# Optimization experiments

Hardware: AMD Instinct MI355X
Metric: run time of the kernel (lower is better)

Reference implementation:

```python
import jax, jax.numpy as jnp
import numpy as np

SIDE = 32
N_NODES = SIDE * SIDE          # n_nodes = 1024
WIDTH = 128
IN_DIM = 128
T_DIM = 2
U_DIM = 1
BATCH = 8
MSG_STEPS = int(np.sqrt(N_NODES))  # 32
LN_EPS = 1e-5


def _create_grid():
    # matches GEN.create_grid for t_dim == 2
    pos = np.array([[i / (SIDE - 1), j / (SIDE - 1)]
                    for i in range(SIDE) for j in range(SIDE)], dtype=np.float32)
    edges = []
    for i in range(1, SIDE):
        for j in range(1, SIDE):
            a = SIDE * i + j
            b = SIDE * (i - 1) + j
            c = SIDE * i + (j - 1)
            edges += [[a, b], [b, a], [c, a], [a, c]]
    edge_index = np.array(edges, dtype=np.int64).T  # [2, E]
    return pos, edge_index


def setup_inputs() -> dict:
    key = jax.random.key(0)
    ks = jax.random.split(key, 16)
    node_pos_np, edge_index_np = _create_grid()

    def lin(k, fan_in, fan_out):
        kw, kb = jax.random.split(k)
        bound = 1.0 / np.sqrt(fan_in)
        W = jax.random.uniform(kw, (fan_in, fan_out), jnp.float32, -bound, bound)
        b = jax.random.uniform(kb, (fan_out,), jnp.float32, -bound, bound)
        return W, b

    We1, be1 = lin(ks[0], IN_DIM, WIDTH)
    We2, be2 = lin(ks[1], WIDTH, WIDTH)
    We3, be3 = lin(ks[2], WIDTH, WIDTH)
    Wg, bg = lin(ks[3], WIDTH + T_DIM, WIDTH)
    Wd1, bd1 = lin(ks[4], WIDTH + T_DIM, WIDTH)
    Wd2, bd2 = lin(ks[5], WIDTH, WIDTH)
    Wd3, bd3 = lin(ks[6], WIDTH, U_DIM)

    return {
        'X1': jax.random.uniform(ks[7], (BATCH, IN_DIM + T_DIM), jnp.float32),
        'node_pos': jnp.asarray(node_pos_np),
        'edge_index': jnp.asarray(edge_index_np),
        'We1': We1, 'be1': be1, 'We2': We2, 'be2': be2, 'We3': We3, 'be3': be3,
        'Wg': Wg, 'bg': bg,
        'gamma': jnp.ones((WIDTH,), jnp.float32),
        'beta': jnp.zeros((WIDTH,), jnp.float32),
        'Wd1': Wd1, 'bd1': bd1, 'Wd2': Wd2, 'bd2': bd2, 'Wd3': Wd3, 'bd3': bd3,
    }


def _gen_forward(X1, node_pos, edge_index, We1, be1, We2, be2, We3, be3,
                 Wg, bg, gamma, beta, Wd1, bd1, Wd2, bd2, Wd3, bd3):
    s, t = X1[:, :-T_DIM], X1[:, -T_DIM:]

    # encoder MLP: Linear-ReLU-Linear-ReLU-Linear
    h = jax.nn.relu(s @ We1 + be1)
    h = jax.nn.relu(h @ We2 + be2)
    enc = h @ We3 + be3                                   # [B, W]

    # per-sample graph construction: softmax over node distance to origin
    # (identical for every sample), node_features = weight @ enc[i][None,:]
    d0 = jnp.sqrt(jnp.sum(node_pos ** 2, axis=1, keepdims=True))  # [N,1]
    w0 = jax.nn.softmax(-d0, axis=0)                              # [N,1]
    x = w0[None, :, :] * enc[:, None, :]                          # [B,N,W]

    # GCNConv normalization with added self-loops (symmetric norm)
    row, col = edge_index[0], edge_index[1]
    deg = jnp.ones((N_NODES,), x.dtype).at[col].add(1.0)
    dinv = deg ** -0.5
    enorm = dinv[row] * dinv[col]   # edge norm
    snorm = dinv * dinv             # self-loop norm
    posb = jnp.broadcast_to(node_pos[None], (x.shape[0], N_NODES, T_DIM))

    def step(xc, _):
        xin = jnp.concatenate([posb, xc], axis=-1)        # [B,N,W+2]
        xw = xin @ Wg                                     # [B,N,W]
        msgs = enorm[None, :, None] * xw[:, row, :]       # [B,E,W]
        agg = (snorm[None, :, None] * xw).at[:, col, :].add(msgs) + bg
        xn = xc + agg
        mu = jnp.mean(xn, axis=-1, keepdims=True)
        var = jnp.var(xn, axis=-1, keepdims=True)
        xn = (xn - mu) * jax.lax.rsqrt(var + LN_EPS) * gamma + beta
        return xn, None

    x, _ = jax.lax.scan(step, x, None, length=MSG_STEPS)  # [B,N,W]

    # readout: softmax over node distance to query point t
    dist = jnp.sqrt(jnp.sum((node_pos[None] - t[:, None, :]) ** 2,
                            axis=2, keepdims=True))       # [B,N,1]
    wt = jax.nn.softmax(-dist, axis=1)                    # [B,N,1]
    hidden = jnp.einsum('bnk,bnw->bw', wt, x)             # [B,W]
    hidden = jnp.concatenate([hidden, t], axis=1)

    h = jax.nn.relu(hidden @ Wd1 + bd1)
    h = jax.nn.relu(h @ Wd2 + bd2)
    y = (h @ Wd3 + bd3).squeeze()                         # [B] (u_dim == 1)
    return y


def reference(X1, node_pos, edge_index, We1, be1, We2, be2, We3, be3,
              Wg, bg, gamma, beta, Wd1, bd1, Wd2, bd2, Wd3, bd3):
    return _gen_forward(X1, node_pos, edge_index, We1, be1, We2, be2, We3, be3,
                        Wg, bg, gamma, beta, Wd1, bd1, Wd2, bd2, Wd3, bd3)
```

## Files before the change

kernel.cpp:

```cpp
#include <hip/hip_runtime.h>

#define NODES 1024
#define WD    128
#define NSTEPS 32
#define LNEPS 1e-5f

typedef __bf16 bf16x8 __attribute__((ext_vector_type(8)));
typedef float  f32x4  __attribute__((ext_vector_type(4)));
typedef int    i32x4  __attribute__((ext_vector_type(4)));

__device__ __forceinline__ f32x4 mfma16(i32x4 a, i32x4 b, f32x4 c) {
  return __builtin_amdgcn_mfma_f32_16x16x32_bf16(
      __builtin_bit_cast(bf16x8, a), __builtin_bit_cast(bf16x8, b), c, 0, 0, 0);
}

__device__ __forceinline__ unsigned short f2bf(float f) {
  union { float f; unsigned u; } v; v.f = f;
  unsigned r = v.u + 0x7FFF + ((v.u >> 16) & 1);
  return (unsigned short)(r >> 16);
}
__device__ __forceinline__ float bf2f(unsigned short h) {
  union { unsigned u; float f; } v; v.u = ((unsigned)h) << 16;
  return v.f;
}

__device__ __forceinline__ float dinv_of(int n) {
  const int i = n >> 5, j = n & 31;
  int cnt = 1;
  cnt += (i >= 1 && j >= 1) ? 1 : 0;
  cnt += (i <= 30 && j >= 1) ? 1 : 0;
  cnt += (i >= 1 && j >= 1) ? 1 : 0;
  cnt += (i >= 1 && j <= 30) ? 1 : 0;
  return 1.f / sqrtf((float)cnt);
}

__device__ __forceinline__ void lay512(const float* __restrict__ W,
                                       const float* __restrict__ bias,
                                       const float* __restrict__ src,
                                       float* __restrict__ dst, int tid,
                                       bool relu_) {
  const int c = tid & 127;
  const int b0 = tid >> 7;
  float a0 = bias ? bias[c] : 0.f;
  float a1 = a0;
#pragma unroll 8
  for (int k = 0; k < WD; k++) {
    const float wv = W[k * WD + c];
    a0 += src[b0 * WD + k] * wv;
    a1 += src[(b0 + 4) * WD + k] * wv;
  }
  dst[b0 * WD + c] = relu_ ? fmaxf(a0, 0.f) : a0;
  dst[(b0 + 4) * WD + c] = relu_ ? fmaxf(a1, 0.f) : a1;
  __syncthreads();
}

__global__ __launch_bounds__(512) void init_kernel(
    const float* __restrict__ X1, const float* __restrict__ pos,
    const float* __restrict__ We1, const float* __restrict__ be1,
    const float* __restrict__ We2, const float* __restrict__ be2,
    const float* __restrict__ We3, const float* __restrict__ be3,
    const float* __restrict__ Wg, const float* __restrict__ bg,
    float* __restrict__ X, float* __restrict__ XW0, float* __restrict__ Q,
    int* __restrict__ Bpk) {
  __shared__ float ioA[1024];
  __shared__ float ioB[1024];
  __shared__ float red[512];
  const int tid = threadIdx.x;
  const int v0 = blockIdx.x * 4;
  const float* W2 = Wg + 2 * WD;

  for (int i = tid; i < 1024; i += 512) ioA[i] = X1[(i >> 7) * 130 + (i & 127)];
  __syncthreads();
  lay512(We1, be1, ioA, ioB, tid, true);
  lay512(We2, be2, ioB, ioA, tid, true);
  lay512(We3, be3, ioA, ioB, tid, false);
  lay512(W2, nullptr, ioB, ioA, tid, false);

  {
    float es = 0.f;
#pragma unroll
    for (int r = 0; r < 2; r++) {
      const int n = tid + 512 * r;
      const float px = pos[2 * n], py = pos[2 * n + 1];
      es += expf(-sqrtf(px * px + py * py));
    }
    red[tid] = es;
  }
  __syncthreads();
  for (int s = 256; s > 0; s >>= 1) {
    if (tid < s) red[tid] += red[tid + s];
    __syncthreads();
  }
  const float w0sum = red[0];

  {
    const int lr = tid >> 4, cq = tid & 15, c0 = cq * 8;
    const int b = lr >> 2, nl = lr & 3, v = v0 + nl;
    const int grow = (b << 10) + v;
    const float pxv = pos[2 * v], pyv = pos[2 * v + 1];
    const float w0v = expf(-sqrtf(pxv * pxv + pyv * pyv)) / w0sum;
#pragma unroll
    for (int q4 = 0; q4 < 2; q4++) {
      const float4 e = *(const float4*)(ioB + b * WD + c0 + 4 * q4);
      const float4 e2 = *(const float4*)(ioA + b * WD + c0 + 4 * q4);
      *(float4*)(X + (size_t)grow * WD + c0 + 4 * q4) =
          make_float4(w0v * e.x, w0v * e.y, w0v * e.z, w0v * e.w);
      *(float4*)(XW0 + (size_t)grow * WD + c0 + 4 * q4) =
          make_float4(w0v * e2.x, w0v * e2.y, w0v * e2.z, w0v * e2.w);
    }
  }
  {
    const int vq = v0 + (tid >> 7);
    const int cc = tid & 127;
    const float dv = dinv_of(vq);
    const float dvv = dv * dv;
    const int iv = vq >> 5, jv = vq & 31;
    float cx = dvv * pos[2 * vq], cy = dvv * pos[2 * vq + 1];
    const bool ex[4] = {(iv >= 1) && (jv >= 1), (iv <= 30) && (jv >= 1),
                        (iv >= 1) && (jv >= 1), (iv >= 1) && (jv <= 30)};
    const int du[4] = {-32, 32, -1, 1};
#pragma unroll
    for (int e = 0; e < 4; e++) {
      if (ex[e]) {
        const int u = vq + du[e];
        const float w = dinv_of(u) * dv;
        cx += w * pos[2 * u];
        cy += w * pos[2 * u + 1];
      }
    }
    Q[vq * WD + cc] = bg[cc] + cx * Wg[cc] + cy * Wg[WD + cc];
  }
  if (tid < 64) {
    const int e = blockIdx.x * 64 + tid;
    const int nt = e >> 11, l = (e >> 5) & 63, half = (e >> 4) & 1;
    const int kt = (e >> 2) & 3, d = e & 3;
    const int k0 = 32 * kt + ((l >> 4) << 3) + 2 * d;
    const int n = 16 * nt + (l & 15);
    const float w0_ = W2[k0 * WD + n];
    const float w1_ = W2[(k0 + 1) * WD + n];
    const unsigned short h0 = f2bf(w0_), h1 = f2bf(w1_);
    int val;
    if (half == 0) {
      val = (int)h0 | ((int)h1 << 16);
    } else {
      val = (int)f2bf(w0_ - bf2f(h0)) | ((int)f2bf(w1_ - bf2f(h1)) << 16);
    }
    Bpk[e] = val;
  }
}

__global__ __launch_bounds__(512) void step_kernel(
    float* __restrict__ X, const float* __restrict__ XWin,
    float* __restrict__ XWout, const int* __restrict__ Bpk,
    const float* __restrict__ Q, const float* __restrict__ gamma,
    const float* __restrict__ beta, const int mode) {
  __shared__ int Ah[32 * 68];
  __shared__ int Al[32 * 68];
  const int tid = threadIdx.x;
  const int v0 = blockIdx.x * 4;
  const int wv = tid >> 6, l = tid & 63;

  i32x4 bh[4], bl[4];
  if (mode) {
    const int lb0 = (wv * 64 + l) * 32;
#pragma unroll
    for (int kt = 0; kt < 4; kt++) {
      bh[kt] = *(const i32x4*)(Bpk + lb0 + kt * 4);
      bl[kt] = *(const i32x4*)(Bpk + lb0 + 16 + kt * 4);
    }
  }

  const int lr = tid >> 4, cq = tid & 15, c0 = cq * 8;
  const int b = lr >> 2, nl = lr & 3, v = v0 + nl;
  const int grow = (b << 10) + v;
  const float dv = dinv_of(v);
  const float dvv = dv * dv;
  const int iv = v >> 5, jv = v & 31;
  const bool ex[4] = {(iv >= 1) && (jv >= 1), (iv <= 30) && (jv >= 1),
                      (iv >= 1) && (jv >= 1), (iv >= 1) && (jv <= 30)};
  const int du[4] = {-32, 32, -1, 1};

  float y[8];
  {
    const float* xr = X + (size_t)grow * WD + c0;
    const float* qr = Q + v * WD + c0;
    const float* wr = XWin + (size_t)grow * WD + c0;
#pragma unroll
    for (int q4 = 0; q4 < 2; q4++) {
      const float4 a = *(const float4*)(xr + 4 * q4);
      const float4 qq = *(const float4*)(qr + 4 * q4);
      const float4 w = *(const float4*)(wr + 4 * q4);
      y[4 * q4 + 0] = a.x + qq.x + dvv * w.x;
      y[4 * q4 + 1] = a.y + qq.y + dvv * w.y;
      y[4 * q4 + 2] = a.z + qq.z + dvv * w.z;
      y[4 * q4 + 3] = a.w + qq.w + dvv * w.w;
    }
  }
#pragma unroll
  for (int e = 0; e < 4; e++) {
    const int u = ex[e] ? v + du[e] : v;
    const float w = ex[e] ? dinv_of(u) * dv : 0.f;
    const float* nr = XWin + (size_t)((b << 10) + u) * WD + c0;
#pragma unroll
    for (int q4 = 0; q4 < 2; q4++) {
      const float4 t = *(const float4*)(nr + 4 * q4);
      y[4 * q4 + 0] += w * t.x;
      y[4 * q4 + 1] += w * t.y;
      y[4 * q4 + 2] += w * t.z;
      y[4 * q4 + 3] += w * t.w;
    }
  }
  float s1 = 0.f, s2 = 0.f;
#pragma unroll
  for (int q = 0; q < 8; q++) { s1 += y[q]; s2 += y[q] * y[q]; }
#pragma unroll
  for (int m = 1; m < 16; m <<= 1) {
    s1 += __shfl_xor(s1, m);
    s2 += __shfl_xor(s2, m);
  }
  const float mu = s1 * (1.f / 128.f);
  const float var = s2 * (1.f / 128.f) - mu * mu;
  const float rs = 1.f / sqrtf(var + LNEPS);
  {
    const float* g4 = gamma + c0;
    const float* b4 = beta + c0;
    float* xo = X + (size_t)grow * WD + c0;
    float xn[8];
#pragma unroll
    for (int q = 0; q < 8; q++) xn[q] = (y[q] - mu) * rs * g4[q] + b4[q];
    *(float4*)(xo) = make_float4(xn[0], xn[1], xn[2], xn[3]);
    *(float4*)(xo + 4) = make_float4(xn[4], xn[5], xn[6], xn[7]);
    if (mode) {
      int hw[4], lw[4];
#pragma unroll
      for (int d = 0; d < 4; d++) {
        const unsigned short ha = f2bf(xn[2 * d]);
        const unsigned short hb = f2bf(xn[2 * d + 1]);
        hw[d] = (int)ha | ((int)hb << 16);
        lw[d] = (int)f2bf(xn[2 * d] - bf2f(ha)) |
                ((int)f2bf(xn[2 * d + 1] - bf2f(hb)) << 16);
      }
      const int abase = lr * 68 + cq * 4;
      *(i32x4*)(Ah + abase) = i32x4{hw[0], hw[1], hw[2], hw[3]};
      *(i32x4*)(Al + abase) = i32x4{lw[0], lw[1], lw[2], lw[3]};
    }
  }

  if (mode) {
    __syncthreads();
    const int g4 = (l >> 4) << 2;
    const int mrow0 = (l & 15) * 68;
    const int mrow1 = mrow0 + 16 * 68;
    f32x4 acc[2] = {};
#pragma unroll
    for (int kt = 0; kt < 4; kt++) {
      const int off = 16 * kt + g4;
      const i32x4 ah0 = *(const i32x4*)(Ah + mrow0 + off);
      const i32x4 ah1 = *(const i32x4*)(Ah + mrow1 + off);
      const i32x4 al0 = *(const i32x4*)(Al + mrow0 + off);
      const i32x4 al1 = *(const i32x4*)(Al + mrow1 + off);
      acc[0] = mfma16(ah0, bh[kt], acc[0]);
      acc[1] = mfma16(ah1, bh[kt], acc[1]);
      acc[0] = mfma16(ah0, bl[kt], acc[0]);
      acc[1] = mfma16(ah1, bl[kt], acc[1]);
      acc[0] = mfma16(al0, bh[kt], acc[0]);
      acc[1] = mfma16(al1, bh[kt], acc[1]);
    }
    const int colb = 16 * wv + (l & 15);
    const int rbase = (l >> 4) << 2;
#pragma unroll
    for (int mt = 0; mt < 2; mt++)
#pragma unroll
      for (int r = 0; r < 4; r++) {
        const int lrr = 16 * mt + rbase + r;
        const int gr = ((lrr >> 2) << 10) + v0 + (lrr & 3);
        XWout[(size_t)gr * WD + colb] = acc[mt][r];
      }
  }
}

__global__ __launch_bounds__(1024) void hiddec_kernel(
    const float* __restrict__ pos, const float* __restrict__ X1,
    const float* __restrict__ Xf, const float* __restrict__ Wd1,
    const float* __restrict__ bd1, const float* __restrict__ Wd2,
    const float* __restrict__ bd2, const float* __restrict__ Wd3,
    const float* __restrict__ bd3, float* __restrict__ out) {
  __shared__ float wsh[NODES];
  __shared__ float red[16];
  __shared__ float asum[8][WD];
  __shared__ float hid[132];
  __shared__ float hh[WD];
  const int b = blockIdx.x;
  const int n = threadIdx.x;
  const float tx = X1[b * 130 + 128], ty = X1[b * 130 + 129];
  const float px = pos[2 * n] - tx, py = pos[2 * n + 1] - ty;
  const float e = expf(-sqrtf(px * px + py * py));
  float s = e;
#pragma unroll
  for (int m = 32; m >= 1; m >>= 1) s += __shfl_xor(s, m);
  if ((n & 63) == 0) red[n >> 6] = s;
  __syncthreads();
  float tot = 0.f;
#pragma unroll
  for (int w = 0; w < 16; w++) tot += red[w];
  wsh[n] = e / tot;
  __syncthreads();
  const int c = n & 127, g = n >> 7;
  {
    const float* xp = Xf + ((size_t)b * NODES + g * 128) * WD + c;
    const float* wp = wsh + g * 128;
    float a = 0.f;
#pragma unroll 4
    for (int it = 0; it < 128; it++) a += wp[it] * xp[it * WD];
    asum[g][c] = a;
  }
  __syncthreads();
  if (g == 0) {
    float t2 = asum[0][c];
#pragma unroll
    for (int gg = 1; gg < 8; gg++) t2 += asum[gg][c];
    hid[c] = t2;
  }
  if (n == 0) { hid[128] = tx; hid[129] = ty; }
  __syncthreads();
  float a1v = 0.f;
  if (n < 128) {
    a1v = bd1[n];
    for (int k = 0; k < 130; k++) a1v += hid[k] * Wd1[k * WD + n];
  }
  __syncthreads();
  if (n < 128) hh[n] = fmaxf(a1v, 0.f);
  __syncthreads();
  float p = 0.f;
  if (n < 128) {
    float a2 = bd2[n];
#pragma unroll 8
    for (int k = 0; k < WD; k++) a2 += hh[k] * Wd2[k * WD + n];
    p = fmaxf(a2, 0.f) * Wd3[n];
  }
#pragma unroll
  for (int m = 32; m >= 1; m >>= 1) p += __shfl_xor(p, m);
  if ((n & 63) == 0) red[n >> 6] = p;
  __syncthreads();
  if (n == 0) out[b] = red[0] + red[1] + bd3[0];
}

extern "C" void kernel_launch(void* const* d_in, const int* in_sizes, int n_in,
                              void* d_out, int out_size, void* d_ws,
                              size_t ws_size, hipStream_t stream) {
  const float* X1 = (const float*)d_in[0];
  const float* pos = (const float*)d_in[1];
  const float* We1 = (const float*)d_in[3];
  const float* be1 = (const float*)d_in[4];
  const float* We2 = (const float*)d_in[5];
  const float* be2 = (const float*)d_in[6];
  const float* We3 = (const float*)d_in[7];
  const float* be3 = (const float*)d_in[8];
  const float* Wg = (const float*)d_in[9];
  const float* bg = (const float*)d_in[10];
  const float* gamma = (const float*)d_in[11];
  const float* beta = (const float*)d_in[12];
  const float* Wd1 = (const float*)d_in[13];
  const float* bd1 = (const float*)d_in[14];
  const float* Wd2 = (const float*)d_in[15];
  const float* bd2 = (const float*)d_in[16];
  const float* Wd3 = (const float*)d_in[17];
  const float* bd3 = (const float*)d_in[18];
  float* out = (float*)d_out;
  float* f = (float*)d_ws;

  float* Q = f;
  int* Bpk = (int*)(f + 131072);
  float* X = f + 147456;
  float* XWa = f + 1196032;
  float* XWb = f + 2244608;

  init_kernel<<<256, 512, 0, stream>>>(X1, pos, We1, be1, We2, be2, We3, be3,
                                       Wg, bg, X, XWa, Q, Bpk);
  for (int t = 0; t < NSTEPS; t++) {
    const float* xin = (t & 1) ? XWb : XWa;
    float* xout = (t & 1) ? XWa : XWb;
    step_kernel<<<256, 512, 0, stream>>>(X, xin, xout, Bpk, Q, gamma, beta,
                                         (t < NSTEPS - 1) ? 1 : 0);
  }
  hiddec_kernel<<<8, 1024, 0, stream>>>(pos, X1, X, Wd1, bd1, Wd2, bd2, Wd3,
                                        bd3, out);
  (void)in_sizes;
  (void)n_in;
  (void)out_size;
  (void)ws_size;
}
```

Before: 263.8 us.

## Fuse all message-passing steps into one persistent kernel with neighbor flags

```diff
diff --git a/kernel.cpp b/kernel.cpp
--- a/kernel.cpp
+++ b/kernel.cpp
@@ -4,6 +4,7 @@
 #define WD    128
 #define NSTEPS 32
 #define LNEPS 1e-5f
+#define FLAGSTRIDE 16
 
 typedef __bf16 bf16x8 __attribute__((ext_vector_type(8)));
 typedef float  f32x4  __attribute__((ext_vector_type(4)));
@@ -22,6 +23,34 @@
 __device__ __forceinline__ float bf2f(unsigned short h) {
   union { unsigned u; float f; } v; v.u = ((unsigned)h) << 16;
   return v.f;
+}
+
+typedef unsigned long long u64;
+__device__ __forceinline__ float2 coh_load2(const float* p) {
+  union { float f[2]; u64 v; } u;
+  u.v = __hip_atomic_load((const u64*)p, __ATOMIC_RELAXED,
+                          __HIP_MEMORY_SCOPE_AGENT);
+  return make_float2(u.f[0], u.f[1]);
+}
+__device__ __forceinline__ void coh_store(float* p, float a) {
+  __hip_atomic_store(p, a, __ATOMIC_RELAXED, __HIP_MEMORY_SCOPE_AGENT);
+}
+
+__device__ __forceinline__ void acc_coh(const float* p, float w,
+                                        float* __restrict__ y) {
+#pragma unroll
+  for (int q = 0; q < 4; q++) {
+    const float2 t = coh_load2(p + 2 * q);
+    y[2 * q] += w * t.x;
+    y[2 * q + 1] += w * t.y;
+  }
+}
+__device__ __forceinline__ void acc_lds(const float* p, float w,
+                                        float* __restrict__ y) {
+  const float4 a = *(const float4*)(p);
+  const float4 b = *(const float4*)(p + 4);
+  y[0] += w * a.x; y[1] += w * a.y; y[2] += w * a.z; y[3] += w * a.w;
+  y[4] += w * b.x; y[5] += w * b.y; y[6] += w * b.z; y[7] += w * b.w;
 }
 
 __device__ __forceinline__ float dinv_of(int n) {
@@ -32,6 +61,21 @@
   cnt += (i >= 1 && j >= 1) ? 1 : 0;
   cnt += (i >= 1 && j <= 30) ? 1 : 0;
   return 1.f / sqrtf((float)cnt);
+}
+
+__device__ __forceinline__ void cvt8(const float* __restrict__ xn, i32x4& hi,
+                                     i32x4& lo) {
+  int hw[4], lw[4];
+#pragma unroll
+  for (int d = 0; d < 4; d++) {
+    const unsigned short ha = f2bf(xn[2 * d]);
+    const unsigned short hb = f2bf(xn[2 * d + 1]);
+    hw[d] = (int)ha | ((int)hb << 16);
+    lw[d] = (int)f2bf(xn[2 * d] - bf2f(ha)) |
+            ((int)f2bf(xn[2 * d + 1] - bf2f(hb)) << 16);
+  }
+  hi = i32x4{hw[0], hw[1], hw[2], hw[3]};
+  lo = i32x4{lw[0], lw[1], lw[2], lw[3]};
 }
 
 __device__ __forceinline__ void lay512(const float* __restrict__ W,
@@ -60,8 +104,7 @@
     const float* __restrict__ We2, const float* __restrict__ be2,
     const float* __restrict__ We3, const float* __restrict__ be3,
     const float* __restrict__ Wg, const float* __restrict__ bg,
-    float* __restrict__ X, float* __restrict__ XW0, float* __restrict__ Q,
-    int* __restrict__ Bpk) {
+    float* __restrict__ X, float* __restrict__ Q, int* __restrict__ Bpk) {
   __shared__ float ioA[1024];
   __shared__ float ioB[1024];
   __shared__ float red[512];
@@ -74,7 +117,6 @@
   lay512(We1, be1, ioA, ioB, tid, true);
   lay512(We2, be2, ioB, ioA, tid, true);
   lay512(We3, be3, ioA, ioB, tid, false);
-  lay512(W2, nullptr, ioB, ioA, tid, false);
 
   {
     float es = 0.f;
@@ -102,11 +144,8 @@
 #pragma unroll
     for (int q4 = 0; q4 < 2; q4++) {
       const float4 e = *(const float4*)(ioB + b * WD + c0 + 4 * q4);
-      const float4 e2 = *(const float4*)(ioA + b * WD + c0 + 4 * q4);
       *(float4*)(X + (size_t)grow * WD + c0 + 4 * q4) =
           make_float4(w0v * e.x, w0v * e.y, w0v * e.z, w0v * e.w);
-      *(float4*)(XW0 + (size_t)grow * WD + c0 + 4 * q4) =
-          make_float4(w0v * e2.x, w0v * e2.y, w0v * e2.z, w0v * e2.w);
     }
   }
   {
@@ -149,19 +188,23 @@
   }
 }
 
-__global__ __launch_bounds__(512) void step_kernel(
-    float* __restrict__ X, const float* __restrict__ XWin,
-    float* __restrict__ XWout, const int* __restrict__ Bpk,
-    const float* __restrict__ Q, const float* __restrict__ gamma,
-    const float* __restrict__ beta, const int mode) {
+__global__ __launch_bounds__(512) void flow_kernel(
+    const float* __restrict__ Xin, float* __restrict__ Xout,
+    float* __restrict__ XWa, float* __restrict__ XWb,
+    const int* __restrict__ Bpk, const float* __restrict__ Q,
+    const float* __restrict__ gamma, const float* __restrict__ beta,
+    int* __restrict__ flags) {
   __shared__ int Ah[32 * 68];
   __shared__ int Al[32 * 68];
+  __shared__ float XWl[32 * 132];
   const int tid = threadIdx.x;
-  const int v0 = blockIdx.x * 4;
+  const int bid = blockIdx.x;
+  const int v0 = bid * 4;
+  const int i0 = v0 >> 5, j0 = v0 & 31;
   const int wv = tid >> 6, l = tid & 63;
 
   i32x4 bh[4], bl[4];
-  if (mode) {
+  {
     const int lb0 = (wv * 64 + l) * 32;
 #pragma unroll
     for (int kt = 0; kt < 4; kt++) {
@@ -171,111 +214,160 @@
   }
 
   const int lr = tid >> 4, cq = tid & 15, c0 = cq * 8;
-  const int b = lr >> 2, nl = lr & 3, v = v0 + nl;
-  const int grow = (b << 10) + v;
+  const int bb = lr >> 2, nl = lr & 3, v = v0 + nl;
+  const int jv = v & 31;
   const float dv = dinv_of(v);
   const float dvv = dv * dv;
-  const int iv = v >> 5, jv = v & 31;
-  const bool ex[4] = {(iv >= 1) && (jv >= 1), (iv <= 30) && (jv >= 1),
-                      (iv >= 1) && (jv >= 1), (iv >= 1) && (jv <= 30)};
-  const int du[4] = {-32, 32, -1, 1};
-
-  float y[8];
-  {
-    const float* xr = X + (size_t)grow * WD + c0;
-    const float* qr = Q + v * WD + c0;
-    const float* wr = XWin + (size_t)grow * WD + c0;
+  const bool upE = (i0 >= 1) && (jv >= 1);
+  const bool dnE = (i0 <= 30) && (jv >= 1);
+  const bool lfE = (i0 >= 1) && (jv >= 1);
+  const bool rtE = (i0 >= 1) && (jv <= 30);
+  const float wUp = upE ? dinv_of(v - 32) * dv : 0.f;
+  const float wDn = dnE ? dinv_of(v + 32) * dv : 0.f;
+  const float wLf = lfE ? dinv_of(v - 1) * dv : 0.f;
+  const float wRt = rtE ? dinv_of(v + 1) * dv : 0.f;
+  const size_t offUp = (size_t)((bb << 10) + (upE ? v - 32 : v)) * WD + c0;
+  const size_t offDn = (size_t)((bb << 10) + (dnE ? v + 32 : v)) * WD + c0;
+  const size_t offLf = (size_t)((bb << 10) + (lfE ? v - 1 : v)) * WD + c0;
+  const size_t offRt = (size_t)((bb << 10) + (rtE ? v + 1 : v)) * WD + c0;
+
+  int nbrB;
+  {
+    const int which = tid;
+    int nb = -1;
+    if (which == 0) nb = (i0 >= 1) ? bid - 8 : -1;
+    if (which == 1) nb = (i0 <= 30) ? bid + 8 : -1;
+    if (which == 2) nb = (i0 >= 1 && j0 >= 1) ? bid - 1 : -1;
+    if (which == 3) nb = (i0 >= 1 && j0 <= 27) ? bid + 1 : -1;
+    nbrB = nb;
+  }
+
+  float x[8], qv[8], gmm[8], btt[8];
+  {
+    const float* xs = Xin + (size_t)((bb << 10) + v) * WD + c0;
+    const float* qs = Q + v * WD + c0;
 #pragma unroll
     for (int q4 = 0; q4 < 2; q4++) {
-      const float4 a = *(const float4*)(xr + 4 * q4);
-      const float4 qq = *(const float4*)(qr + 4 * q4);
-      const float4 w = *(const float4*)(wr + 4 * q4);
-      y[4 * q4 + 0] = a.x + qq.x + dvv * w.x;
-      y[4 * q4 + 1] = a.y + qq.y + dvv * w.y;
-      y[4 * q4 + 2] = a.z + qq.z + dvv * w.z;
-      y[4 * q4 + 3] = a.w + qq.w + dvv * w.w;
-    }
-  }
-#pragma unroll
-  for (int e = 0; e < 4; e++) {
-    const int u = ex[e] ? v + du[e] : v;
-    const float w = ex[e] ? dinv_of(u) * dv : 0.f;
-    const float* nr = XWin + (size_t)((b << 10) + u) * WD + c0;
-#pragma unroll
-    for (int q4 = 0; q4 < 2; q4++) {
-      const float4 t = *(const float4*)(nr + 4 * q4);
-      y[4 * q4 + 0] += w * t.x;
-      y[4 * q4 + 1] += w * t.y;
-      y[4 * q4 + 2] += w * t.z;
-      y[4 * q4 + 3] += w * t.w;
-    }
-  }
-  float s1 = 0.f, s2 = 0.f;
-#pragma unroll
-  for (int q = 0; q < 8; q++) { s1 += y[q]; s2 += y[q] * y[q]; }
-#pragma unroll
-  for (int m = 1; m < 16; m <<= 1) {
-    s1 += __shfl_xor(s1, m);
-    s2 += __shfl_xor(s2, m);
-  }
-  const float mu = s1 * (1.f / 128.f);
-  const float var = s2 * (1.f / 128.f) - mu * mu;
-  const float rs = 1.f / sqrtf(var + LNEPS);
-  {
-    const float* g4 = gamma + c0;
-    const float* b4 = beta + c0;
-    float* xo = X + (size_t)grow * WD + c0;
-    float xn[8];
-#pragma unroll
-    for (int q = 0; q < 8; q++) xn[q] = (y[q] - mu) * rs * g4[q] + b4[q];
-    *(float4*)(xo) = make_float4(xn[0], xn[1], xn[2], xn[3]);
-    *(float4*)(xo + 4) = make_float4(xn[4], xn[5], xn[6], xn[7]);
-    if (mode) {
-      int hw[4], lw[4];
-#pragma unroll
-      for (int d = 0; d < 4; d++) {
-        const unsigned short ha = f2bf(xn[2 * d]);
-        const unsigned short hb = f2bf(xn[2 * d + 1]);
-        hw[d] = (int)ha | ((int)hb << 16);
-        lw[d] = (int)f2bf(xn[2 * d] - bf2f(ha)) |
-                ((int)f2bf(xn[2 * d + 1] - bf2f(hb)) << 16);
-      }
-      const int abase = lr * 68 + cq * 4;
-      *(i32x4*)(Ah + abase) = i32x4{hw[0], hw[1], hw[2], hw[3]};
-      *(i32x4*)(Al + abase) = i32x4{lw[0], lw[1], lw[2], lw[3]};
-    }
-  }
-
-  if (mode) {
+      const float4 a = *(const float4*)(xs + 4 * q4);
+      const float4 qq = *(const float4*)(qs + 4 * q4);
+      const float4 gg = *(const float4*)(gamma + c0 + 4 * q4);
+      const float4 be = *(const float4*)(beta + c0 + 4 * q4);
+      x[4 * q4 + 0] = a.x; x[4 * q4 + 1] = a.y;
+      x[4 * q4 + 2] = a.z; x[4 * q4 + 3] = a.w;
+      qv[4 * q4 + 0] = qq.x; qv[4 * q4 + 1] = qq.y;
+      qv[4 * q4 + 2] = qq.z; qv[4 * q4 + 3] = qq.w;
+      gmm[4 * q4 + 0] = gg.x; gmm[4 * q4 + 1] = gg.y;
+      gmm[4 * q4 + 2] = gg.z; gmm[4 * q4 + 3] = gg.w;
+      btt[4 * q4 + 0] = be.x; btt[4 * q4 + 1] = be.y;
+      btt[4 * q4 + 2] = be.z; btt[4 * q4 + 3] = be.w;
+    }
+  }
+  {
+    i32x4 hi, lo;
+    cvt8(x, hi, lo);
+    const int ab = lr * 68 + cq * 4;
+    *(i32x4*)(Ah + ab) = hi;
+    *(i32x4*)(Al + ab) = lo;
+  }
+
+  const int g4 = (l >> 4) << 2;
+  const int mr0 = (l & 15) * 68;
+  const int mr1 = mr0 + 16 * 68;
+  const int colb = 16 * wv + (l & 15);
+  const int rbase = (l >> 4) << 2;
+
+  for (int t = 0; t < NSTEPS; t++) {
+    float* __restrict__ xw = (t & 1) ? XWb : XWa;
     __syncthreads();
-    const int g4 = (l >> 4) << 2;
-    const int mrow0 = (l & 15) * 68;
-    const int mrow1 = mrow0 + 16 * 68;
-    f32x4 acc[2] = {};
+    f32x4 acc0 = {}, acc1 = {};
 #pragma unroll
     for (int kt = 0; kt < 4; kt++) {
       const int off = 16 * kt + g4;
-      const i32x4 ah0 = *(const i32x4*)(Ah + mrow0 + off);
-      const i32x4 ah1 = *(const i32x4*)(Ah + mrow1 + off);
-      const i32x4 al0 = *(const i32x4*)(Al + mrow0 + off);
-      const i32x4 al1 = *(const i32x4*)(Al + mrow1 + off);
-      acc[0] = mfma16(ah0, bh[kt], acc[0]);
-      acc[1] = mfma16(ah1, bh[kt], acc[1]);
-      acc[0] = mfma16(ah0, bl[kt], acc[0]);
-      acc[1] = mfma16(ah1, bl[kt], acc[1]);
-      acc[0] = mfma16(al0, bh[kt], acc[0]);
-      acc[1] = mfma16(al1, bh[kt], acc[1]);
-    }
-    const int colb = 16 * wv + (l & 15);
-    const int rbase = (l >> 4) << 2;
-#pragma unroll
-    for (int mt = 0; mt < 2; mt++)
-#pragma unroll
-      for (int r = 0; r < 4; r++) {
-        const int lrr = 16 * mt + rbase + r;
-        const int gr = ((lrr >> 2) << 10) + v0 + (lrr & 3);
-        XWout[(size_t)gr * WD + colb] = acc[mt][r];
+      const i32x4 ah0 = *(const i32x4*)(Ah + mr0 + off);
+      const i32x4 ah1 = *(const i32x4*)(Ah + mr1 + off);
+      const i32x4 al0 = *(const i32x4*)(Al + mr0 + off);
+      const i32x4 al1 = *(const i32x4*)(Al + mr1 + off);
+      acc0 = mfma16(ah0, bh[kt], acc0);
+      acc1 = mfma16(ah1, bh[kt], acc1);
+      acc0 = mfma16(ah0, bl[kt], acc0);
+      acc1 = mfma16(ah1, bl[kt], acc1);
+      acc0 = mfma16(al0, bh[kt], acc0);
+      acc1 = mfma16(al1, bh[kt], acc1);
+    }
+#pragma unroll
+    for (int r = 0; r < 4; r++) {
+      const int lr0 = rbase + r, lr1 = 16 + rbase + r;
+      XWl[lr0 * 132 + colb] = acc0[r];
+      XWl[lr1 * 132 + colb] = acc1[r];
+      const int g0 = ((lr0 >> 2) << 10) + v0 + (lr0 & 3);
+      const int g1 = ((lr1 >> 2) << 10) + v0 + (lr1 & 3);
+      coh_store(xw + (size_t)g0 * WD + colb, acc0[r]);
+      coh_store(xw + (size_t)g1 * WD + colb, acc1[r]);
+    }
+    __syncthreads();
+    if (tid == 0)
+      __hip_atomic_store(flags + bid * FLAGSTRIDE, t + 1, __ATOMIC_RELEASE,
+                         __HIP_MEMORY_SCOPE_AGENT);
+    if (tid < 4 && nbrB >= 0) {
+      const int* fp = flags + nbrB * FLAGSTRIDE;
+      int cap = 0;
+      while (__hip_atomic_load(fp, __ATOMIC_ACQUIRE,
+                               __HIP_MEMORY_SCOPE_AGENT) < t + 1) {
+        __builtin_amdgcn_s_sleep(4);
+        if (++cap > 2000000) break;
       }
+    }
+    __syncthreads();
+
+    float y[8];
+    {
+      const float* s = XWl + lr * 132 + c0;
+      const float4 w0v = *(const float4*)(s);
+      const float4 w1v = *(const float4*)(s + 4);
+      y[0] = x[0] + qv[0] + dvv * w0v.x;
+      y[1] = x[1] + qv[1] + dvv * w0v.y;
+      y[2] = x[2] + qv[2] + dvv * w0v.z;
+      y[3] = x[3] + qv[3] + dvv * w0v.w;
+      y[4] = x[4] + qv[4] + dvv * w1v.x;
+      y[5] = x[5] + qv[5] + dvv * w1v.y;
+      y[6] = x[6] + qv[6] + dvv * w1v.z;
+      y[7] = x[7] + qv[7] + dvv * w1v.w;
+    }
+    if (upE) acc_coh(xw + offUp, wUp, y);
+    if (dnE) acc_coh(xw + offDn, wDn, y);
+    if (lfE) {
+      if (nl > 0) acc_lds(XWl + (lr - 1) * 132 + c0, wLf, y);
+      else acc_coh(xw + offLf, wLf, y);
+    }
+    if (rtE) {
+      if (nl < 3) acc_lds(XWl + (lr + 1) * 132 + c0, wRt, y);
+      else acc_coh(xw + offRt, wRt, y);
+    }
+    float s1 = 0.f, s2 = 0.f;
+#pragma unroll
+    for (int q = 0; q < 8; q++) { s1 += y[q]; s2 += y[q] * y[q]; }
+#pragma unroll
+    for (int m = 1; m < 16; m <<= 1) {
+      s1 += __shfl_xor(s1, m);
+      s2 += __shfl_xor(s2, m);
+    }
+    const float mu = s1 * (1.f / 128.f);
+    const float var = s2 * (1.f / 128.f) - mu * mu;
+    const float rs = 1.f / sqrtf(var + LNEPS);
+#pragma unroll
+    for (int q = 0; q < 8; q++) x[q] = (y[q] - mu) * rs * gmm[q] + btt[q];
+    {
+      i32x4 hi, lo;
+      cvt8(x, hi, lo);
+      const int ab = lr * 68 + cq * 4;
+      *(i32x4*)(Ah + ab) = hi;
+      *(i32x4*)(Al + ab) = lo;
+    }
+  }
+  {
+    float* xo = Xout + (size_t)((bb << 10) + v) * WD + c0;
+    *(float4*)(xo) = make_float4(x[0], x[1], x[2], x[3]);
+    *(float4*)(xo + 4) = make_float4(x[4], x[5], x[6], x[7]);
   }
 }
 
@@ -369,21 +461,20 @@
   float* out = (float*)d_out;
   float* f = (float*)d_ws;
 
-  float* Q = f;
-  int* Bpk = (int*)(f + 131072);
-  float* X = f + 147456;
-  float* XWa = f + 1196032;
-  float* XWb = f + 2244608;
-
+  int* flags = (int*)d_ws;
+  float* Q = f + 4096;
+  int* Bpk = (int*)(f + 135168);
+  float* Xa = f + 151552;
+  float* Xb = f + 1200128;
+  float* XWa = f + 2248704;
+  float* XWb = f + 3297280;
+
+  hipMemsetAsync(flags, 0, 4096 * sizeof(int), stream);
   init_kernel<<<256, 512, 0, stream>>>(X1, pos, We1, be1, We2, be2, We3, be3,
-                                       Wg, bg, X, XWa, Q, Bpk);
-  for (int t = 0; t < NSTEPS; t++) {
-    const float* xin = (t & 1) ? XWb : XWa;
-    float* xout = (t & 1) ? XWa : XWb;
-    step_kernel<<<256, 512, 0, stream>>>(X, xin, xout, Bpk, Q, gamma, beta,
-                                         (t < NSTEPS - 1) ? 1 : 0);
-  }
-  hiddec_kernel<<<8, 1024, 0, stream>>>(pos, X1, X, Wd1, bd1, Wd2, bd2, Wd3,
+                                       Wg, bg, Xa, Q, Bpk);
+  flow_kernel<<<256, 512, 0, stream>>>(Xa, Xb, XWa, XWb, Bpk, Q, gamma, beta,
+                                       flags);
+  hiddec_kernel<<<8, 1024, 0, stream>>>(pos, X1, Xb, Wd1, bd1, Wd2, bd2, Wd3,
                                         bd3, out);
   (void)in_sizes;
   (void)n_in;
```

After: 335.5 us. +27.2%, slower.
